# Kernel tuning notes

Measured on AMD Instinct MI355X. Metric: run time of the kernel, lower is better.

The kernel has to match this reference:

```python
import jax, jax.numpy as jnp
import numpy as np

N_NODES, D = 10000, 128
N_EDGES = 640000
BN_EPS = 1e-3  # keras BatchNormalization default


def _bn(x, gamma, beta, mean, var):
    return (x - mean) * jax.lax.rsqrt(var + BN_EPS) * gamma + beta


def _ffn_block(x, gamma, beta, mean, var, W, b):
    # BatchNorm (inference) -> Dropout (identity at inference) -> Dense + gelu (exact, keras default)
    return jax.nn.gelu(_bn(x, gamma, beta, mean, var) @ W + b, approximate=False)


def setup_inputs() -> dict:
    key = jax.random.key(0)
    ks = jax.random.split(key, 32)
    inp = {
        "node_features": jax.random.normal(ks[0], (N_NODES, D), jnp.float32),
        "edges": jax.random.randint(ks[1], (2, N_EDGES), 0, N_NODES, jnp.int64),
        "edge_weights": jax.random.uniform(ks[2], (N_EDGES,), jnp.float32),
    }
    def bn_params(i, dim, prefix):
        return {
            prefix + "_g": jnp.ones((dim,), jnp.float32) + 0.1 * jax.random.normal(ks[i], (dim,)),
            prefix + "_b": 0.1 * jax.random.normal(ks[i + 1], (dim,)),
            prefix + "_m": 0.1 * jax.random.normal(ks[i + 2], (dim,)),
            prefix + "_v": jax.random.uniform(ks[i + 3], (dim,), minval=0.5, maxval=1.5),
        }
    def dense_params(i, din, dout, prefix):
        s = (2.0 / (din + dout)) ** 0.5
        return {
            prefix + "_W": s * jax.random.normal(ks[i], (din, dout), jnp.float32),
            prefix + "_bias": jnp.zeros((dout,), jnp.float32),
        }
    # prepare FFN: BN(D)->Dense(D->128), BN(128)->Dense(128->128)
    inp.update(bn_params(3, D, "p1")); inp.update(dense_params(7, D, 128, "p1"))
    inp.update(bn_params(8, 128, "p2")); inp.update(dense_params(12, 128, 128, "p2"))
    # update FFN (concat -> 2*D input): BN(2D)->Dense(2D->128), BN(128)->Dense(128->128)
    inp.update(bn_params(13, 2 * D, "u1")); inp.update(dense_params(17, 2 * D, 128, "u1"))
    inp.update(bn_params(18, 128, "u2")); inp.update(dense_params(22, 128, 128, "u2"))
    return inp


def reference(node_features, edges, edge_weights,
              p1_g, p1_b, p1_m, p1_v, p1_W, p1_bias,
              p2_g, p2_b, p2_m, p2_v, p2_W, p2_bias,
              u1_g, u1_b, u1_m, u1_v, u1_W, u1_bias,
              u2_g, u2_b, u2_m, u2_v, u2_W, u2_bias):
    num_nodes = node_features.shape[0]
    node_idx, nbr_idx = edges[0], edges[1]
    # gather neighbor representations [E, D]
    neigh = node_features[nbr_idx]
    # prepare: ffn on neighbors, then scale by edge weights
    msg = _ffn_block(neigh, p1_g, p1_b, p1_m, p1_v, p1_W, p1_bias)
    msg = _ffn_block(msg, p2_g, p2_b, p2_m, p2_v, p2_W, p2_bias)
    msg = msg * edge_weights[:, None]
    # aggregate: unsorted_segment_mean
    agg = jax.ops.segment_sum(msg, node_idx, num_segments=num_nodes)
    cnt = jax.ops.segment_sum(jnp.ones_like(edge_weights), node_idx, num_segments=num_nodes)
    agg = agg / jnp.maximum(cnt, 1.0)[:, None]
    # update: concat + ffn
    h = jnp.concatenate([node_features, agg], axis=1)
    h = _ffn_block(h, u1_g, u1_b, u1_m, u1_v, u1_W, u1_bias)
    h = _ffn_block(h, u2_g, u2_b, u2_m, u2_v, u2_W, u2_bias)
    return h
```

## Files before the change

kernel.cpp:

```cpp
#include <hip/hip_runtime.h>
#include <hip/hip_bf16.h>
#include <hip/hip_fp16.h>
#include <math.h>

#define N_NODES 10000
#define DIM 128
#define N_EDGES 640000
#define BN_EPS 1e-3f

#define QUARTER 2500
#define QPAD 3072
#define PART_BLOCKS 250
#define EDGES_PER_PART 2560
#define SCAT_GRID 1000
#define MSG64_BLOCKS 157
#define SU_BLOCKS 1250

typedef _Float16 half8 __attribute__((ext_vector_type(8)));
typedef float f32x4 __attribute__((ext_vector_type(4)));

__device__ __forceinline__ float gelu_exact(float x) {
  return 0.5f * x * (1.0f + erff(x * 0.70710678f));
}

__device__ __forceinline__ int lds_swz(int row, int colbyte) {
  return ((row * 256 + colbyte) ^ ((row & 7) << 4));
}

__device__ __forceinline__ unsigned char f32_to_fp8(float v) {
  unsigned pk = __builtin_amdgcn_cvt_pk_fp8_f32(v, v, 0, false);
  return (unsigned char)(pk & 0xffu);
}

struct FoldAll {
  const float* g[4];
  const float* bb[4];
  const float* m[4];
  const float* v[4];
  const float* W[4];
  const float* bias[4];
  _Float16* pk[4];
  float* bf[4];
  int din[4];
  int S[4];
};

__global__ __launch_bounds__(256) void fold_hist_kernel(FoldAll fa,
                                                        const int* __restrict__ node_idx,
                                                        unsigned char* __restrict__ part,
                                                        int* __restrict__ histq,
                                                        int* __restrict__ qtot) {
  __shared__ int lh[N_NODES];
  __shared__ float t_sh[256];
  __shared__ float bpart[128];
  int b = blockIdx.x, t = threadIdx.x;
  if (b >= 44) {
    int eb = b - 44;
    for (int i = t; i < N_NODES; i += 256) lh[i] = 0;
    __syncthreads();
    int base0 = eb * EDGES_PER_PART;
#pragma unroll
    for (int s = 0; s < 3; ++s) {
      int off = s * 1024 + t * 4;
      if (off < EDGES_PER_PART) {
        int4 vv = *reinterpret_cast<const int4*>(&node_idx[base0 + off]);
        atomicAdd(&lh[vv.x], 1);
        atomicAdd(&lh[vv.y], 1);
        atomicAdd(&lh[vv.z], 1);
        atomicAdd(&lh[vv.w], 1);
      }
    }
    __syncthreads();
    for (int i = t; i < N_NODES; i += 256) {
      int q = i / QUARTER;
      int bp = i - q * QUARTER;
      part[(size_t)(q * PART_BLOCKS + eb) * QUARTER + bp] = (unsigned char)lh[i];
    }
    return;
  }
  if (b >= 40) {
    int p = b - 40;
    if (p == 0 && t < 4) qtot[t] = 0;
    for (int i = t; i < QPAD - QUARTER; i += 256) histq[p * QPAD + QUARTER + i] = 0;
    int din = fa.din[p];
    const float* W = fa.W[p];
    for (int k = t; k < din; k += 256) {
      float sc = fa.g[p][k] * rsqrtf(fa.v[p][k] + BN_EPS);
      t_sh[k] = fa.bb[p][k] - fa.m[p][k] * sc;
    }
    __syncthreads();
    int j = t & 127, kh = t >> 7;
    int half = din >> 1;
    float acc = 0.f;
    for (int k = kh * half; k < (kh + 1) * half; ++k)
      acc = fmaf(t_sh[k], W[k * 128 + j], acc);
    if (kh == 1) bpart[j] = acc;
    __syncthreads();
    if (kh == 0) fa.bf[p][j] = acc + bpart[j] + fa.bias[p][j];
    return;
  }
  int p, lf;
  if (b < 8)       { p = 0; lf = b * 256 + t; }
  else if (b < 16) { p = 1; lf = (b - 8) * 256 + t; }
  else if (b < 32) { p = 2; lf = (b - 16) * 256 + t; }
  else             { p = 3; lf = (b - 32) * 256 + t; }
  int S = fa.S[p];
  int l = lf & 63;
  int fs = lf >> 6;
  int f = fs & 7, s = fs >> 3;
  if (s >= S) return;
  const float* W = fa.W[p];
  const float* g = fa.g[p];
  const float* v = fa.v[p];
  int k0 = s * 32 + (l >> 4) * 8;
  int col = f * 16 + (l & 15);
  half8 h;
#pragma unroll
  for (int i = 0; i < 8; ++i) {
    int k = k0 + i;
    float sc = g[k] * rsqrtf(v[k] + BN_EPS);
    h[i] = (_Float16)(sc * W[k * 128 + col]);
  }
  *reinterpret_cast<half8*>(fa.pk[p] + (size_t)lf * 8) = h;
}

__global__ __launch_bounds__(256) void merge_msg_kernel(
    unsigned char* __restrict__ part, int* __restrict__ histq,
    int* __restrict__ qtot,
    const float* __restrict__ x,
    const _Float16* __restrict__ W1pk, const float* __restrict__ b1f,
    const _Float16* __restrict__ W2pk, const float* __restrict__ b2f,
    unsigned char* __restrict__ M8) {
  __shared__ char lds_raw[4 * 4096];
  __shared__ int qsum[4];
  int b = blockIdx.x, t = threadIdx.x;
  if (b < 40) {
    int bin = b * 256 + t;
    int sum = 0;
    int q = 0;
    if (bin < N_NODES) {
      q = bin / QUARTER;
      int bp = bin - q * QUARTER;
      unsigned char* col = part + (size_t)q * PART_BLOCKS * QUARTER + bp;
#pragma unroll
      for (int c = 0; c < PART_BLOCKS; c += 25) {
        int vals[25];
#pragma unroll
        for (int i = 0; i < 25; ++i) vals[i] = col[(size_t)(c + i) * QUARTER];
#pragma unroll
        for (int i = 0; i < 25; ++i) {
          col[(size_t)(c + i) * QUARTER] = (unsigned char)sum;
          sum += vals[i];
        }
      }
      histq[q * QPAD + bp] = sum;
    }
    if (t < 4) qsum[t] = 0;
    __syncthreads();
    if (bin < N_NODES) atomicAdd(&qsum[q], sum);
    __syncthreads();
    if (t < 4) atomicAdd(&qtot[t], qsum[t]);
    return;
  }
  int wid = t >> 6, lane = t & 63;
  int r = lane & 15, g = lane >> 4;
  int row0 = (b - 40) * 64 + wid * 16;
  char* lbase = lds_raw + wid * 4096;

  int arow = row0 + r;
  if (arow > N_NODES - 1) arow = N_NODES - 1;
  const float* xp = x + (size_t)arow * DIM;

  half8 a[4];
#pragma unroll
  for (int s = 0; s < 4; ++s) {
    float4 lo = *reinterpret_cast<const float4*>(xp + s * 32 + g * 8);
    float4 hi = *reinterpret_cast<const float4*>(xp + s * 32 + g * 8 + 4);
    half8 h;
    h[0] = (_Float16)lo.x; h[1] = (_Float16)lo.y; h[2] = (_Float16)lo.z; h[3] = (_Float16)lo.w;
    h[4] = (_Float16)hi.x; h[5] = (_Float16)hi.y; h[6] = (_Float16)hi.z; h[7] = (_Float16)hi.w;
    a[s] = h;
  }

  f32x4 zero = {0.f, 0.f, 0.f, 0.f};
  f32x4 acc[8];
#pragma unroll
  for (int f = 0; f < 8; ++f) acc[f] = zero;
#pragma unroll
  for (int f = 0; f < 8; ++f)
#pragma unroll
    for (int s = 0; s < 4; ++s) {
      half8 bfrag = *reinterpret_cast<const half8*>(W1pk + (size_t)((s * 8 + f) * 64 + lane) * 8);
      acc[f] = __builtin_amdgcn_mfma_f32_16x16x32_f16(a[s], bfrag, acc[f], 0, 0, 0);
    }

#pragma unroll
  for (int f = 0; f < 8; ++f) {
    int col = f * 16 + r;
    float bv = b1f[col];
#pragma unroll
    for (int j = 0; j < 4; ++j) {
      int rl = g * 4 + j;
      float gv = gelu_exact(acc[f][j] + bv);
      *reinterpret_cast<_Float16*>(lbase + lds_swz(rl, col * 2)) = (_Float16)gv;
    }
  }

  half8 a2[4];
#pragma unroll
  for (int s = 0; s < 4; ++s)
    a2[s] = *reinterpret_cast<const half8*>(lbase + lds_swz(r, (s * 32 + g * 8) * 2));

  f32x4 acc2[8];
#pragma unroll
  for (int f = 0; f < 8; ++f) acc2[f] = zero;
#pragma unroll
  for (int f = 0; f < 8; ++f)
#pragma unroll
    for (int s = 0; s < 4; ++s) {
      half8 bfrag = *reinterpret_cast<const half8*>(W2pk + (size_t)((s * 8 + f) * 64 + lane) * 8);
      acc2[f] = __builtin_amdgcn_mfma_f32_16x16x32_f16(a2[s], bfrag, acc2[f], 0, 0, 0);
    }

#pragma unroll
  for (int f = 0; f < 8; ++f) {
    int col = f * 16 + r;
    float bv = b2f[col];
#pragma unroll
    for (int j = 0; j < 4; ++j) {
      int grow = row0 + g * 4 + j;
      if (grow < N_NODES)
        M8[(size_t)grow * DIM + col] = f32_to_fp8(gelu_exact(acc2[f][j] + bv));
    }
  }
}

__global__ __launch_bounds__(256) void scatter_kernel(
    const int* __restrict__ node_idx, const int* __restrict__ nbr_idx,
    const float* __restrict__ ew, const int* __restrict__ histq,
    const int* __restrict__ qtot,
    const unsigned char* __restrict__ part, uint2* __restrict__ edge_s,
    int* __restrict__ row_start) {
  __shared__ int cur[QUARTER];
  __shared__ int sums[256];
  int bk = blockIdx.x, t = threadIdx.x;
  int eb = bk >> 2;
  int q = bk & 3;
  int qbase = q * QUARTER;
  const int PER = 12;
  int i0 = t * PER;
  const int* hq = histq + q * QPAD;
  int lh[PER];
  int total = 0;
#pragma unroll
  for (int i = 0; i < PER; i += 4) {
    int4 h4 = *reinterpret_cast<const int4*>(&hq[i0 + i]);
    lh[i] = h4.x; lh[i + 1] = h4.y; lh[i + 2] = h4.z; lh[i + 3] = h4.w;
    total += h4.x + h4.y + h4.z + h4.w;
  }
  sums[t] = total;
  __syncthreads();
  for (int off = 1; off < 256; off <<= 1) {
    int v = (t >= off) ? sums[t - off] : 0;
    __syncthreads();
    sums[t] += v;
    __syncthreads();
  }
  int q0 = qtot[0], q1 = qtot[1], q2 = qtot[2];
  int qpre = (q >= 1 ? q0 : 0) + (q >= 2 ? q1 : 0) + (q >= 3 ? q2 : 0);
  int running = qpre + sums[t] - total;
  const unsigned char* prow = part + (size_t)(q * PART_BLOCKS + eb) * QUARTER;
  bool wrs = (eb == 0);
#pragma unroll
  for (int i = 0; i < PER; ++i) {
    int idx = i0 + i;
    if (idx < QUARTER) {
      cur[idx] = running + (int)prow[idx];
      if (wrs) row_start[qbase + idx] = running;
      running += lh[i];
    }
  }
  if (bk == 0 && t == 0) row_start[N_NODES] = N_EDGES;
  __syncthreads();

  int base0 = eb * EDGES_PER_PART;
#pragma unroll
  for (int s = 0; s < 3; ++s) {
    int off = s * 1024 + t * 4;
    if (off >= EDGES_PER_PART) break;
    int base = base0 + off;
    int4 ni = *reinterpret_cast<const int4*>(&node_idx[base]);
    int4 nb = *reinterpret_cast<const int4*>(&nbr_idx[base]);
    float4 wv = *reinterpret_cast<const float4*>(&ew[base]);
    unsigned d0 = (unsigned)(ni.x - qbase);
    unsigned d1 = (unsigned)(ni.y - qbase);
    unsigned d2 = (unsigned)(ni.z - qbase);
    unsigned d3 = (unsigned)(ni.w - qbase);
    if (d0 < QUARTER) {
      int p0 = atomicAdd(&cur[d0], 1);
      edge_s[p0] = make_uint2((unsigned)nb.x, __float_as_uint(wv.x));
    }
    if (d1 < QUARTER) {
      int p1 = atomicAdd(&cur[d1], 1);
      edge_s[p1] = make_uint2((unsigned)nb.y, __float_as_uint(wv.y));
    }
    if (d2 < QUARTER) {
      int p2 = atomicAdd(&cur[d2], 1);
      edge_s[p2] = make_uint2((unsigned)nb.z, __float_as_uint(wv.z));
    }
    if (d3 < QUARTER) {
      int p3 = atomicAdd(&cur[d3], 1);
      edge_s[p3] = make_uint2((unsigned)nb.w, __float_as_uint(wv.w));
    }
  }
}

__global__ __launch_bounds__(256) void spmm_update_kernel(
    const int* __restrict__ row_start, const uint2* __restrict__ edge_s,
    const unsigned char* __restrict__ M8, const float* __restrict__ x,
    const _Float16* __restrict__ U1pk, const float* __restrict__ bu1,
    const _Float16* __restrict__ U2pk, const float* __restrict__ bu2,
    float* __restrict__ out) {
  __shared__ float scratch[3][8][128];
  __shared__ char tile[4096];
  int t = threadIdx.x;
  int row0 = blockIdx.x * 8;

  {
    int r = t >> 5;
    int q = t & 31;
    int slice = q >> 3;
    int sub = q & 7;
    int row = row0 + r;
    int s = row_start[row];
    int e_end = row_start[row + 1];
    float acc[16];
#pragma unroll
    for (int c = 0; c < 16; ++c) acc[c] = 0.f;
    const unsigned char* Mb = M8 + sub * 16;
    int base = s + slice * 4;
    uint2 pk[4];
#pragma unroll
    for (int k = 0; k < 4; ++k) {
      int e = base + k;
      pk[k] = edge_s[(e < e_end) ? e : s];
      if (e >= e_end) pk[k].y = 0u;
    }
    for (; base < e_end; base += 16) {
      uint2 pkn[4];
      int nb = base + 16;
#pragma unroll
      for (int k = 0; k < 4; ++k) {
        int e = nb + k;
        pkn[k] = edge_s[(e < e_end) ? e : s];
        if (e >= e_end) pkn[k].y = 0u;
      }
      uint4 raw[4];
#pragma unroll
      for (int k = 0; k < 4; ++k)
        raw[k] = *reinterpret_cast<const uint4*>(Mb + (size_t)pk[k].x * DIM);
#pragma unroll
      for (int k = 0; k < 4; ++k) {
        float w = __uint_as_float(pk[k].y);
        const unsigned* u32s = reinterpret_cast<const unsigned*>(&raw[k]);
#pragma unroll
        for (int qq = 0; qq < 4; ++qq) {
          auto f01 = __builtin_amdgcn_cvt_pk_f32_fp8(u32s[qq], false);
          auto f23 = __builtin_amdgcn_cvt_pk_f32_fp8(u32s[qq], true);
          acc[4 * qq + 0] = fmaf(w, f01[0], acc[4 * qq + 0]);
          acc[4 * qq + 1] = fmaf(w, f01[1], acc[4 * qq + 1]);
          acc[4 * qq + 2] = fmaf(w, f23[0], acc[4 * qq + 2]);
          acc[4 * qq + 3] = fmaf(w, f23[1], acc[4 * qq + 3]);
        }
      }
#pragma unroll
      for (int k = 0; k < 4; ++k) pk[k] = pkn[k];
    }
    if (slice >= 1) {
      float* dst = &scratch[slice - 1][r][sub * 16];
      *reinterpret_cast<float4*>(dst) = make_float4(acc[0], acc[1], acc[2], acc[3]);
      *reinterpret_cast<float4*>(dst + 4) = make_float4(acc[4], acc[5], acc[6], acc[7]);
      *reinterpret_cast<float4*>(dst + 8) = make_float4(acc[8], acc[9], acc[10], acc[11]);
      *reinterpret_cast<float4*>(dst + 12) = make_float4(acc[12], acc[13], acc[14], acc[15]);
    }
    __syncthreads();
    if (slice == 0) {
#pragma unroll
      for (int sl = 0; sl < 3; ++sl) {
        const float* src = &scratch[sl][r][sub * 16];
#pragma unroll
        for (int c = 0; c < 16; c += 4) {
          float4 o = *reinterpret_cast<const float4*>(src + c);
          acc[c] += o.x; acc[c + 1] += o.y; acc[c + 2] += o.z; acc[c + 3] += o.w;
        }
      }
      int cnt = e_end - s;
      float inv = 1.f / (float)(cnt > 0 ? cnt : 1);
      half8 hlo, hhi;
#pragma unroll
      for (int c = 0; c < 8; ++c) hlo[c] = (_Float16)(acc[c] * inv);
#pragma unroll
      for (int c = 0; c < 8; ++c) hhi[c] = (_Float16)(acc[8 + c] * inv);
      *reinterpret_cast<half8*>(tile + lds_swz(r, sub * 32)) = hlo;
      *reinterpret_cast<half8*>(tile + lds_swz(r, sub * 32 + 16)) = hhi;
    }
  }
  __syncthreads();

  int wid = t >> 6, lane = t & 63;
  int r = lane & 15, g = lane >> 4;
  half8 hzero;
#pragma unroll
  for (int i = 0; i < 8; ++i) hzero[i] = (_Float16)0.f;

  half8 a[8];
#pragma unroll
  for (int s = 0; s < 8; ++s) a[s] = hzero;
  if (r < 8) {
    const float* xp = x + (size_t)(row0 + r) * DIM;
#pragma unroll
    for (int s = 0; s < 4; ++s) {
      float4 lo = *reinterpret_cast<const float4*>(xp + s * 32 + g * 8);
      float4 hi = *reinterpret_cast<const float4*>(xp + s * 32 + g * 8 + 4);
      half8 h;
      h[0] = (_Float16)lo.x; h[1] = (_Float16)lo.y; h[2] = (_Float16)lo.z; h[3] = (_Float16)lo.w;
      h[4] = (_Float16)hi.x; h[5] = (_Float16)hi.y; h[6] = (_Float16)hi.z; h[7] = (_Float16)hi.w;
      a[s] = h;
    }
#pragma unroll
    for (int s = 0; s < 4; ++s)
      a[4 + s] = *reinterpret_cast<const half8*>(tile + lds_swz(r, (s * 32 + g * 8) * 2));
  }
  __syncthreads();

  f32x4 zero = {0.f, 0.f, 0.f, 0.f};
  {
    f32x4 acc1[2];
    acc1[0] = zero; acc1[1] = zero;
#pragma unroll
    for (int fi = 0; fi < 2; ++fi) {
      int f = wid * 2 + fi;
#pragma unroll
      for (int s = 0; s < 8; ++s) {
        half8 bfrag = *reinterpret_cast<const half8*>(U1pk + (size_t)((s * 8 + f) * 64 + lane) * 8);
        acc1[fi] = __builtin_amdgcn_mfma_f32_16x16x32_f16(a[s], bfrag, acc1[fi], 0, 0, 0);
      }
    }
#pragma unroll
    for (int fi = 0; fi < 2; ++fi) {
      int f = wid * 2 + fi;
      int col = f * 16 + r;
      float bv = bu1[col];
#pragma unroll
      for (int j = 0; j < 4; ++j) {
        int rl = g * 4 + j;
        float gv = gelu_exact(acc1[fi][j] + bv);
        *reinterpret_cast<_Float16*>(tile + lds_swz(rl, col * 2)) = (_Float16)gv;
      }
    }
  }
  __syncthreads();

  {
    half8 a2[4];
#pragma unroll
    for (int s = 0; s < 4; ++s) a2[s] = hzero;
    if (r < 8) {
#pragma unroll
      for (int s = 0; s < 4; ++s)
        a2[s] = *reinterpret_cast<const half8*>(tile + lds_swz(r, (s * 32 + g * 8) * 2));
    }
    f32x4 acc2[2];
    acc2[0] = zero; acc2[1] = zero;
#pragma unroll
    for (int fi = 0; fi < 2; ++fi) {
      int f = wid * 2 + fi;
#pragma unroll
      for (int s = 0; s < 4; ++s) {
        half8 bfrag = *reinterpret_cast<const half8*>(U2pk + (size_t)((s * 8 + f) * 64 + lane) * 8);
        acc2[fi] = __builtin_amdgcn_mfma_f32_16x16x32_f16(a2[s], bfrag, acc2[fi], 0, 0, 0);
      }
    }
#pragma unroll
    for (int fi = 0; fi < 2; ++fi) {
      int f = wid * 2 + fi;
      int col = f * 16 + r;
      float bv = bu2[col];
#pragma unroll
      for (int j = 0; j < 4; ++j) {
        int rloc = g * 4 + j;
        if (rloc < 8)
          out[(size_t)(row0 + rloc) * DIM + col] = gelu_exact(acc2[fi][j] + bv);
      }
    }
  }
}

extern "C" void kernel_launch(void* const* d_in, const int* in_sizes, int n_in,
                              void* d_out, int out_size, void* d_ws, size_t ws_size,
                              hipStream_t stream) {
  const float* x = (const float*)d_in[0];
  const int* edges = (const int*)d_in[1];
  const float* ew = (const float*)d_in[2];

  const int* node_idx = edges;
  const int* nbr_idx = edges + N_EDGES;

  char* wsp = (char*)d_ws;
  auto alloc = [&](size_t bytes) {
    char* p = wsp;
    wsp += (bytes + 255) & ~(size_t)255;
    return p;
  };
  unsigned char* M8 = (unsigned char*)alloc((size_t)N_NODES * DIM);
  _Float16* W1pk = (_Float16*)alloc(128 * 128 * 2);
  _Float16* W2pk = (_Float16*)alloc(128 * 128 * 2);
  _Float16* U1pk = (_Float16*)alloc(256 * 128 * 2);
  _Float16* U2pk = (_Float16*)alloc(128 * 128 * 2);
  float* b1f = (float*)alloc(128 * 4);
  float* b2f = (float*)alloc(128 * 4);
  float* bu1 = (float*)alloc(128 * 4);
  float* bu2 = (float*)alloc(128 * 4);
  int* histq = (int*)alloc(4 * QPAD * 4);
  int* qtot = (int*)alloc(4 * 4);
  int* row_start = (int*)alloc((N_NODES + 1) * 4);
  unsigned char* part = (unsigned char*)alloc((size_t)PART_BLOCKS * N_NODES);
  uint2* edge_s = (uint2*)alloc((size_t)N_EDGES * 8);

  FoldAll fa;
  fa.g[0] = (const float*)d_in[3];  fa.bb[0] = (const float*)d_in[4];
  fa.m[0] = (const float*)d_in[5];  fa.v[0] = (const float*)d_in[6];
  fa.W[0] = (const float*)d_in[7];  fa.bias[0] = (const float*)d_in[8];
  fa.g[1] = (const float*)d_in[9];  fa.bb[1] = (const float*)d_in[10];
  fa.m[1] = (const float*)d_in[11]; fa.v[1] = (const float*)d_in[12];
  fa.W[1] = (const float*)d_in[13]; fa.bias[1] = (const float*)d_in[14];
  fa.g[2] = (const float*)d_in[15]; fa.bb[2] = (const float*)d_in[16];
  fa.m[2] = (const float*)d_in[17]; fa.v[2] = (const float*)d_in[18];
  fa.W[2] = (const float*)d_in[19]; fa.bias[2] = (const float*)d_in[20];
  fa.g[3] = (const float*)d_in[21]; fa.bb[3] = (const float*)d_in[22];
  fa.m[3] = (const float*)d_in[23]; fa.v[3] = (const float*)d_in[24];
  fa.W[3] = (const float*)d_in[25]; fa.bias[3] = (const float*)d_in[26];
  fa.pk[0] = W1pk; fa.pk[1] = W2pk; fa.pk[2] = U1pk; fa.pk[3] = U2pk;
  fa.bf[0] = b1f; fa.bf[1] = b2f; fa.bf[2] = bu1; fa.bf[3] = bu2;
  fa.din[0] = 128; fa.din[1] = 128; fa.din[2] = 256; fa.din[3] = 128;
  fa.S[0] = 4; fa.S[1] = 4; fa.S[2] = 8; fa.S[3] = 4;

  fold_hist_kernel<<<44 + PART_BLOCKS, 256, 0, stream>>>(fa, node_idx, part, histq, qtot);
  merge_msg_kernel<<<40 + MSG64_BLOCKS, 256, 0, stream>>>(
      part, histq, qtot, x, W1pk, b1f, W2pk, b2f, M8);
  scatter_kernel<<<SCAT_GRID, 256, 0, stream>>>(
      node_idx, nbr_idx, ew, histq, qtot, part, edge_s, row_start);
  spmm_update_kernel<<<SU_BLOCKS, 256, 0, stream>>>(
      row_start, edge_s, M8, x, U1pk, bu1, U2pk, bu2, (float*)d_out);
}
```

Measured before the change: 95.77 us.

## Pack edge index and bf16 weight into 32 bits; halve histogram LDS

```diff
diff --git a/kernel.cpp b/kernel.cpp
--- a/kernel.cpp
+++ b/kernel.cpp
@@ -30,6 +30,10 @@
 __device__ __forceinline__ unsigned char f32_to_fp8(float v) {
   unsigned pk = __builtin_amdgcn_cvt_pk_fp8_f32(v, v, 0, false);
   return (unsigned char)(pk & 0xffu);
+}
+
+__device__ __forceinline__ unsigned pack_edge(int nbr, float w) {
+  return ((unsigned)nbr << 16) | ((__float_as_uint(w) + 0x8000u) >> 16);
 }
 
 struct FoldAll {
@@ -50,13 +54,13 @@
                                                         unsigned char* __restrict__ part,
                                                         int* __restrict__ histq,
                                                         int* __restrict__ qtot) {
-  __shared__ int lh[N_NODES];
+  __shared__ int lh2[N_NODES / 2];
   __shared__ float t_sh[256];
   __shared__ float bpart[128];
   int b = blockIdx.x, t = threadIdx.x;
   if (b >= 44) {
     int eb = b - 44;
-    for (int i = t; i < N_NODES; i += 256) lh[i] = 0;
+    for (int i = t; i < N_NODES / 2; i += 256) lh2[i] = 0;
     __syncthreads();
     int base0 = eb * EDGES_PER_PART;
 #pragma unroll
@@ -64,17 +68,18 @@
       int off = s * 1024 + t * 4;
       if (off < EDGES_PER_PART) {
         int4 vv = *reinterpret_cast<const int4*>(&node_idx[base0 + off]);
-        atomicAdd(&lh[vv.x], 1);
-        atomicAdd(&lh[vv.y], 1);
-        atomicAdd(&lh[vv.z], 1);
-        atomicAdd(&lh[vv.w], 1);
+        atomicAdd(&lh2[vv.x >> 1], 1 << ((vv.x & 1) << 4));
+        atomicAdd(&lh2[vv.y >> 1], 1 << ((vv.y & 1) << 4));
+        atomicAdd(&lh2[vv.z >> 1], 1 << ((vv.z & 1) << 4));
+        atomicAdd(&lh2[vv.w >> 1], 1 << ((vv.w & 1) << 4));
       }
     }
     __syncthreads();
     for (int i = t; i < N_NODES; i += 256) {
+      int c = (lh2[i >> 1] >> ((i & 1) << 4)) & 0xFFFF;
       int q = i / QUARTER;
       int bp = i - q * QUARTER;
-      part[(size_t)(q * PART_BLOCKS + eb) * QUARTER + bp] = (unsigned char)lh[i];
+      part[(size_t)(q * PART_BLOCKS + eb) * QUARTER + bp] = (unsigned char)c;
     }
     return;
   }
@@ -239,7 +244,7 @@
     const int* __restrict__ node_idx, const int* __restrict__ nbr_idx,
     const float* __restrict__ ew, const int* __restrict__ histq,
     const int* __restrict__ qtot,
-    const unsigned char* __restrict__ part, uint2* __restrict__ edge_s,
+    const unsigned char* __restrict__ part, unsigned* __restrict__ edge_s,
     int* __restrict__ row_start) {
   __shared__ int cur[QUARTER];
   __shared__ int sums[256];
@@ -298,25 +303,25 @@
     unsigned d3 = (unsigned)(ni.w - qbase);
     if (d0 < QUARTER) {
       int p0 = atomicAdd(&cur[d0], 1);
-      edge_s[p0] = make_uint2((unsigned)nb.x, __float_as_uint(wv.x));
+      edge_s[p0] = pack_edge(nb.x, wv.x);
     }
     if (d1 < QUARTER) {
       int p1 = atomicAdd(&cur[d1], 1);
-      edge_s[p1] = make_uint2((unsigned)nb.y, __float_as_uint(wv.y));
+      edge_s[p1] = pack_edge(nb.y, wv.y);
     }
     if (d2 < QUARTER) {
       int p2 = atomicAdd(&cur[d2], 1);
-      edge_s[p2] = make_uint2((unsigned)nb.z, __float_as_uint(wv.z));
+      edge_s[p2] = pack_edge(nb.z, wv.z);
     }
     if (d3 < QUARTER) {
       int p3 = atomicAdd(&cur[d3], 1);
-      edge_s[p3] = make_uint2((unsigned)nb.w, __float_as_uint(wv.w));
+      edge_s[p3] = pack_edge(nb.w, wv.w);
     }
   }
 }
 
 __global__ __launch_bounds__(256) void spmm_update_kernel(
-    const int* __restrict__ row_start, const uint2* __restrict__ edge_s,
+    const int* __restrict__ row_start, const unsigned* __restrict__ edge_s,
     const unsigned char* __restrict__ M8, const float* __restrict__ x,
     const _Float16* __restrict__ U1pk, const float* __restrict__ bu1,
     const _Float16* __restrict__ U2pk, const float* __restrict__ bu2,
@@ -339,29 +344,29 @@
     for (int c = 0; c < 16; ++c) acc[c] = 0.f;
     const unsigned char* Mb = M8 + sub * 16;
     int base = s + slice * 4;
-    uint2 pk[4];
+    unsigned pk[4];
 #pragma unroll
     for (int k = 0; k < 4; ++k) {
       int e = base + k;
       pk[k] = edge_s[(e < e_end) ? e : s];
-      if (e >= e_end) pk[k].y = 0u;
+      if (e >= e_end) pk[k] &= 0xFFFF0000u;
     }
     for (; base < e_end; base += 16) {
-      uint2 pkn[4];
+      unsigned pkn[4];
       int nb = base + 16;
 #pragma unroll
       for (int k = 0; k < 4; ++k) {
         int e = nb + k;
         pkn[k] = edge_s[(e < e_end) ? e : s];
-        if (e >= e_end) pkn[k].y = 0u;
+        if (e >= e_end) pkn[k] &= 0xFFFF0000u;
       }
       uint4 raw[4];
 #pragma unroll
       for (int k = 0; k < 4; ++k)
-        raw[k] = *reinterpret_cast<const uint4*>(Mb + (size_t)pk[k].x * DIM);
+        raw[k] = *reinterpret_cast<const uint4*>(Mb + (size_t)(pk[k] >> 16) * DIM);
 #pragma unroll
       for (int k = 0; k < 4; ++k) {
-        float w = __uint_as_float(pk[k].y);
+        float w = __uint_as_float(pk[k] << 16);
         const unsigned* u32s = reinterpret_cast<const unsigned*>(&raw[k]);
 #pragma unroll
         for (int qq = 0; qq < 4; ++qq) {
@@ -525,7 +530,7 @@
   int* qtot = (int*)alloc(4 * 4);
   int* row_start = (int*)alloc((N_NODES + 1) * 4);
   unsigned char* part = (unsigned char*)alloc((size_t)PART_BLOCKS * N_NODES);
-  uint2* edge_s = (uint2*)alloc((size_t)N_EDGES * 8);
+  unsigned* edge_s = (unsigned*)alloc((size_t)N_EDGES * 4);
 
   FoldAll fa;
   fa.g[0] = (const float*)d_in[3];  fa.bb[0] = (const float*)d_in[4];
```

Measured after the change: 94.62 us. No clear change (-1.2%).
